# Kernel optimization log

Measured on AMD Instinct MI355X. Metric: run time of the kernel, lower is better.

Reference implementation:

```python
import jax, jax.numpy as jnp
import numpy as np

B, T, N, C = 1, 8, 1152, 768
H, DH = 12, 64          # attention heads / head dim; also RG-LRU block-diagonal heads
MLP = 3072
LRU = 768
CONV_W = 4              # recurrentgemma temporal conv width
N_IMG = 1024            # image tokens blocked by mask_image2image


def rms_norm(x, scale):
    var = jnp.mean(jnp.square(x), axis=-1, keepdims=True)
    return x * jax.lax.rsqrt(var + 1e-6) * (1.0 + scale)


def layer_norm(x, scale, bias):
    m = jnp.mean(x, axis=-1, keepdims=True)
    v = jnp.var(x, axis=-1, keepdims=True)
    return (x - m) * jax.lax.rsqrt(v + 1e-6) * scale + bias


def block_diag_linear(x, w, b):
    # x [..., LRU] -> per-head block-diagonal linear (recurrentgemma BlockDiagonalLinear)
    xs = x.reshape(x.shape[:-1] + (H, DH))
    y = jnp.einsum('...hd,hde->...he', xs, w) + b
    return y.reshape(x.shape)


def setup_inputs():
    key = jax.random.key(0)
    ks = jax.random.split(key, 24)
    def nrm(k, shape, s=0.02):
        return jax.random.normal(k, shape, jnp.float32) * s
    return dict(
        x=jax.random.normal(ks[0], (B, T, N, C), jnp.float32),
        tpre_scale=nrm(ks[1], (C,)),
        w_y=nrm(ks[2], (C, LRU)), b_y=jnp.zeros((LRU,)),
        w_x=nrm(ks[3], (C, LRU)), b_x=jnp.zeros((LRU,)),
        conv_w=nrm(ks[4], (CONV_W, LRU)), conv_b=jnp.zeros((LRU,)),
        a_param=jax.random.uniform(ks[5], (LRU,), jnp.float32, 1.0, 4.0),
        ig_w=nrm(ks[6], (H, DH, DH)), ig_b=jnp.zeros((H, DH)),
        ag_w=nrm(ks[7], (H, DH, DH)), ag_b=jnp.zeros((H, DH)),
        w_out=nrm(ks[8], (LRU, C)), b_out=jnp.zeros((C,)),
        cpre_scale=nrm(ks[9], (C,)),
        ffw_up_w=nrm(ks[10], (2, C, MLP)), ffw_up_b=jnp.zeros((2, MLP)),
        ffw_down_w=nrm(ks[11], (MLP, C)), ffw_down_b=jnp.zeros((C,)),
        ln1_s=jnp.ones((C,)), ln1_b=jnp.zeros((C,)),
        wq=nrm(ks[12], (C, H, DH)), bq=jnp.zeros((H, DH)),
        wk=nrm(ks[13], (C, H, DH)), bk=jnp.zeros((H, DH)),
        wv=nrm(ks[14], (C, H, DH)), bv=jnp.zeros((H, DH)),
        wo=nrm(ks[15], (H, DH, C)), bo=jnp.zeros((C,)),
        ln2_s=jnp.ones((C,)), ln2_b=jnp.zeros((C,)),
        mlp_w1=nrm(ks[16], (C, MLP)), mlp_b1=jnp.zeros((MLP,)),
        mlp_w2=nrm(ks[17], (MLP, C)), mlp_b2=jnp.zeros((C,)),
    )


def forward(x, tpre_scale, w_y, b_y, w_x, b_x, conv_w, conv_b, a_param,
            ig_w, ig_b, ag_w, ag_b, w_out, b_out, cpre_scale,
            ffw_up_w, ffw_up_b, ffw_down_w, ffw_down_b,
            ln1_s, ln1_b, wq, bq, wk, bk, wv, bv, wo, bo,
            ln2_s, ln2_b, mlp_w1, mlp_b1, mlp_w2, mlp_b2):
    b, t, n, c = x.shape
    # ---- temporal RG-LRU residual block over time: [(b t) n c] -> [(b n) t c] ----
    xt = x.transpose(0, 2, 1, 3).reshape(b * n, t, c)
    raw = xt
    xn = rms_norm(xt, tpre_scale)
    y = jax.nn.gelu(xn @ w_y + b_y)              # gate branch
    u = xn @ w_x + b_x                           # recurrent branch
    # causal depthwise temporal conv (width 4)
    up = jnp.pad(u, ((0, 0), (CONV_W - 1, 0), (0, 0)))
    u = sum(conv_w[i] * up[:, i:i + t] for i in range(CONV_W)) + conv_b
    # RG-LRU
    gate_x = jax.nn.sigmoid(block_diag_linear(u, ig_w, ig_b))
    gate_a = jax.nn.sigmoid(block_diag_linear(u, ag_w, ag_b))
    log_a = -8.0 * gate_a * jax.nn.softplus(a_param)
    a = jnp.exp(log_a)                           # [bn, t, LRU]
    mult = jnp.sqrt(jnp.maximum(1.0 - jnp.exp(2.0 * log_a), 0.0))
    reset = (jnp.arange(t) == 0)[None, :, None]
    mult = jnp.where(reset, 1.0, mult)
    a = jnp.where(reset, 0.0, a)
    norm_x = u * gate_x * mult
    def step(h, inputs):
        a_t, x_t = inputs
        h = a_t * h + x_t
        return h, h
    _, hs = jax.lax.scan(step, jnp.zeros((b * n, LRU), u.dtype),
                         (a.transpose(1, 0, 2), norm_x.transpose(1, 0, 2)))
    h = hs.transpose(1, 0, 2)                    # [bn, t, LRU]
    s = (h * y) @ w_out + b_out
    resid = s + raw
    # gated MLP (recurrentgemma MLPBlock)
    z = rms_norm(resid, cpre_scale)
    up2 = jnp.einsum('btd,cdD->cbtD', z, ffw_up_w) + ffw_up_b[:, None, None, :]
    z = (jax.nn.gelu(up2[0]) * up2[1]) @ ffw_down_w + ffw_down_b
    xt = z + resid
    # ---- spatial ViT block over tokens: back to [(b t) n c] ----
    xs = xt.reshape(b, n, t, c).transpose(0, 2, 1, 3).reshape(b * t, n, c)
    y1 = layer_norm(xs, ln1_s, ln1_b)
    q = jnp.einsum('bnc,chd->bnhd', y1, wq) + bq
    k = jnp.einsum('bnc,chd->bnhd', y1, wk) + bk
    v = jnp.einsum('bnc,chd->bnhd', y1, wv) + bv
    logits = jnp.einsum('bqhd,bkhd->bhqk', q, k) / jnp.sqrt(jnp.asarray(DH, q.dtype))
    # mask_image2image: image tokens (first 1024) cannot attend to image tokens
    mask = jnp.ones((n, n), bool).at[:N_IMG, :N_IMG].set(False)
    logits = jnp.where(mask[None, None], logits, jnp.finfo(logits.dtype).min)
    attn = jax.nn.softmax(logits, axis=-1)
    sa = jnp.einsum('bhqk,bkhd->bqhd', attn, v)
    sa = jnp.einsum('bqhd,hdc->bqc', sa, wo) + bo
    xs = xs + sa
    y2 = layer_norm(xs, ln2_s, ln2_b)
    m = jax.nn.gelu(y2 @ mlp_w1 + mlp_b1) @ mlp_w2 + mlp_b2
    xs = xs + m
    return xs.reshape(b, t, n, c)


def reference(x, tpre_scale, w_y, b_y, w_x, b_x, conv_w, conv_b, a_param,
              ig_w, ig_b, ag_w, ag_b, w_out, b_out, cpre_scale,
              ffw_up_w, ffw_up_b, ffw_down_w, ffw_down_b,
              ln1_s, ln1_b, wq, bq, wk, bk, wv, bv, wo, bo,
              ln2_s, ln2_b, mlp_w1, mlp_b1, mlp_w2, mlp_b2):
    return forward(x, tpre_scale, w_y, b_y, w_x, b_x, conv_w, conv_b, a_param,
                   ig_w, ig_b, ag_w, ag_b, w_out, b_out, cpre_scale,
                   ffw_up_w, ffw_up_b, ffw_down_w, ffw_down_b,
                   ln1_s, ln1_b, wq, bq, wk, bk, wv, bv, wo, bo,
                   ln2_s, ln2_b, mlp_w1, mlp_b1, mlp_w2, mlp_b2)
```

## Files before the change

kernel.cpp:

```cpp
#include <hip/hip_runtime.h>
#include <hip/hip_bf16.h>

typedef __hip_bfloat16 bf16;
typedef __attribute__((ext_vector_type(4))) float f32x4;
typedef __attribute__((ext_vector_type(8))) short short8;
typedef __attribute__((ext_vector_type(4))) short s16x4;

#define T_ 8
#define N_ 1152
#define C_ 768
#define H_ 12
#define DH_ 64
#define MLP_ 3072
#define LRU_ 768
#define NIMG_ 1024
#define M_ (T_*N_)

__device__ __forceinline__ float b2f(bf16 v){ return __bfloat162float(v); }
__device__ __forceinline__ bf16  f2b(float f){ return __float2bfloat16(f); }
__device__ __forceinline__ float bfs(short u){ return __uint_as_float(((unsigned int)(unsigned short)u) << 16); }
__device__ __forceinline__ float gelu_tanh(float x){
  float x3 = x*x*x;
  float z = 1.5957691216057308f*(x + 0.044715f*x3);
  float e = __expf(z);
  float t = 1.f - 2.f/(e + 1.f);
  return 0.5f*x*(1.f + t);
}
__device__ __forceinline__ void gll16(const void* g, void* l) {
  __builtin_amdgcn_global_load_lds((const __attribute__((address_space(1))) void*)g,
                                   (__attribute__((address_space(3))) void*)l, 16, 0, 0);
}
__device__ __forceinline__ f32x4 mfma16(short8 a, short8 b, f32x4 c) {
  return __builtin_amdgcn_mfma_f32_16x16x32_bf16(a, b, c, 0, 0, 0);
}

__global__ __launch_bounds__(256)
void convertT(const float* __restrict__ W, bf16* __restrict__ Wt, int Kd, int Nd,
              int rs, int ro) {
  __shared__ float tile[64][65];
  int k0 = blockIdx.y * 64, n0 = blockIdx.x * 64;
  int tid = threadIdx.x;
  int c = tid & 63, rr = tid >> 6;
  #pragma unroll
  for (int i = 0; i < 16; i++) {
    int r = rr * 16 + i;
    tile[r][c] = W[(size_t)(k0 + r) * Nd + n0 + c];
  }
  __syncthreads();
  #pragma unroll
  for (int i = 0; i < 16; i++) {
    int n = rr * 16 + i;
    Wt[(size_t)((n0 + n) * rs + ro) * Kd + k0 + c] = f2b(tile[c][n]);
  }
}

struct CvJob  { const float* src; bf16* dst; };
struct CvJobs { CvJob j[4]; };
__global__ __launch_bounds__(256)
void convertT4(CvJobs jobs, int Kd, int Nd, int rs, int zro) {
  __shared__ float tile[64][65];
  int z = blockIdx.z;
  const float* __restrict__ W  = jobs.j[z].src;
  bf16* __restrict__ Wt        = jobs.j[z].dst;
  int ro = z * zro;
  int k0 = blockIdx.y * 64, n0 = blockIdx.x * 64;
  int tid = threadIdx.x;
  int c = tid & 63, rr = tid >> 6;
  #pragma unroll
  for (int i = 0; i < 16; i++) {
    int r = rr * 16 + i;
    tile[r][c] = W[(size_t)(k0 + r) * Nd + n0 + c];
  }
  __syncthreads();
  #pragma unroll
  for (int i = 0; i < 16; i++) {
    int n = rr * 16 + i;
    Wt[(size_t)((n0 + n) * rs + ro) * Kd + k0 + c] = f2b(tile[c][n]);
  }
}

__global__ __launch_bounds__(256)
void convert_gw(const float* __restrict__ igw, const float* __restrict__ agw,
                const float* __restrict__ igb, const float* __restrict__ agb,
                bf16* __restrict__ GW, float* __restrict__ GB) {
  int h = blockIdx.x;
  for (int idx = threadIdx.x; idx < 128 * 64; idx += 256) {
    int rowc = idx >> 6;
    int d    = idx & 63;
    int e    = rowc >> 1;
    const float* W = (rowc & 1) ? agw : igw;
    GW[((size_t)h * 128 + rowc) * 64 + d] = f2b(W[((size_t)h * 64 + d) * 64 + e]);
  }
  if (threadIdx.x < 128) {
    int rowc = threadIdx.x;
    GB[h * 128 + rowc] = ((rowc & 1) ? agb : igb)[h * 64 + (rowc >> 1)];
  }
}

template<int EPI, int ACT>
__global__ __launch_bounds__(256)
void mgemm(const bf16* __restrict__ A, const bf16* __restrict__ Wt,
           const float* __restrict__ bias, const float* __restrict__ bias2,
           void* __restrict__ outp, int K, int Nd) {
  __shared__ bf16 As[2][128][32];
  __shared__ bf16 Bs[2][128][32];
  int tid = threadIdx.x;
  int wave = tid >> 6, lane = tid & 63;
  int wm = wave >> 1, wn = wave & 1;
  int ln15 = lane & 15, quad = lane >> 4;
  int row0 = blockIdx.y * 128, col0 = blockIdx.x * 128;
  const bf16* ag = A  + (size_t)(row0 + wave*32 + (lane>>2)) * K + (lane&3)*8;
  const bf16* bg = Wt + (size_t)(col0 + wave*32 + (lane>>2)) * K + (lane&3)*8;
  f32x4 zero = {0.f, 0.f, 0.f, 0.f};
  f32x4 acc[4][4];
  #pragma unroll
  for (int i = 0; i < 4; i++)
    #pragma unroll
    for (int j = 0; j < 4; j++) acc[i][j] = zero;

  gll16(ag,          &As[0][wave*32][0]);
  gll16(ag + 16*K,   &As[0][wave*32 + 16][0]);
  gll16(bg,          &Bs[0][wave*32][0]);
  gll16(bg + 16*K,   &Bs[0][wave*32 + 16][0]);
  __syncthreads();

  int nt = K >> 5;
  int cur = 0;
  for (int t = 0; t < nt; ++t) {
    if (t + 1 < nt) {
      int k1 = (t + 1) << 5;
      gll16(ag + k1,          &As[cur^1][wave*32][0]);
      gll16(ag + 16*K + k1,   &As[cur^1][wave*32 + 16][0]);
      gll16(bg + k1,          &Bs[cur^1][wave*32][0]);
      gll16(bg + 16*K + k1,   &Bs[cur^1][wave*32 + 16][0]);
    }
    short8 af[4], bf[4];
    #pragma unroll
    for (int i = 0; i < 4; i++)
      af[i] = *(const short8*)&As[cur][wm*64 + i*16 + ln15][quad*8];
    #pragma unroll
    for (int i = 0; i < 4; i++)
      bf[i] = *(const short8*)&Bs[cur][wn*64 + i*16 + ln15][quad*8];
    #pragma unroll
    for (int i = 0; i < 4; i++)
      #pragma unroll
      for (int j = 0; j < 4; j++)
        acc[i][j] = mfma16(af[i], bf[j], acc[i][j]);
    __syncthreads();
    cur ^= 1;
  }

  #pragma unroll
  for (int i = 0; i < 4; i++) {
    #pragma unroll
    for (int j = 0; j < 4; j++) {
      int col = col0 + wn*64 + j*16 + ln15;
      float bv;
      if (EPI == 3)      bv = bias[(col & 1) * (Nd >> 1) + (col >> 1)];
      else if (EPI == 4) bv = (col < (Nd >> 1)) ? bias[col] : bias2[col - (Nd >> 1)];
      else               bv = bias[col];
      #pragma unroll
      for (int r = 0; r < 4; r++) {
        int row = row0 + wm*64 + i*16 + quad*4 + r;
        float v = acc[i][j][r] + bv;
        if (EPI == 3) {
          float pv = __shfl_xor(v, 1, 64);
          if ((lane & 1) == 0)
            ((bf16*)outp)[(size_t)row * (Nd >> 1) + (col >> 1)] = f2b(gelu_tanh(v) * pv);
        } else if (EPI == 4) {
          if (ACT && col < (Nd >> 1)) v = gelu_tanh(v);
          ((bf16*)outp)[(size_t)row * Nd + col] = f2b(v);
        } else {
          if (ACT) v = gelu_tanh(v);
          if (EPI == 0) {
            ((bf16*)outp)[(size_t)row * Nd + col] = f2b(v);
          } else if (EPI == 1) {
            size_t o = (size_t)row * Nd + col;
            ((float*)outp)[o] = v + bias2[o];
          } else if (EPI == 2) {
            int tt = row / N_; int nn = row - tt * N_;
            ((bf16*)outp)[(((size_t)tt * H_ + (col >> 6)) * 64 + (col & 63)) * N_ + nn] = f2b(v);
          }
        }
      }
    }
  }
}

template<int LN>
__global__ __launch_bounds__(256)
void norm_kernel(const float* __restrict__ inp, const float* __restrict__ s,
                 const float* __restrict__ b, bf16* __restrict__ out) {
  int wid  = threadIdx.x >> 6;
  int lane = threadIdx.x & 63;
  int tok  = blockIdx.x * 4 + wid;
  const float* ip = inp + (size_t)tok*C_ + lane*4;
  f32x4 v[3];
  float sum = 0.f, sq = 0.f;
  #pragma unroll
  for (int i = 0; i < 3; i++) {
    v[i] = *(const f32x4*)(ip + i*256);
    #pragma unroll
    for (int j = 0; j < 4; j++) { sum += v[i][j]; sq += v[i][j]*v[i][j]; }
  }
  #pragma unroll
  for (int o = 32; o > 0; o >>= 1) {
    sum += __shfl_xor(sum, o, 64);
    sq  += __shfl_xor(sq, o, 64);
  }
  float scale, mean = 0.f;
  if (LN) {
    mean = sum * (1.f / C_);
    float var = sq * (1.f / C_) - mean * mean;
    scale = rsqrtf(var + 1e-6f);
  } else {
    scale = rsqrtf(sq * (1.f / C_) + 1e-6f);
  }
  #pragma unroll
  for (int i = 0; i < 3; i++) {
    int c0 = i*256 + lane*4;
    f32x4 sc = *(const f32x4*)(s + c0);
    f32x4 bb;
    if (LN) bb = *(const f32x4*)(b + c0);
    bf16 tmp[4];
    #pragma unroll
    for (int j = 0; j < 4; j++) {
      float r;
      if (LN) r = (v[i][j] - mean) * scale * sc[j] + bb[j];
      else    r = v[i][j] * scale * (1.f + sc[j]);
      tmp[j] = f2b(r);
    }
    *(s16x4*)(out + (size_t)tok*C_ + c0) = *(const s16x4*)tmp;
  }
}

__global__ __launch_bounds__(256)
void conv_kernel(const bf16* __restrict__ u0, const float* __restrict__ cw,
                 const float* __restrict__ cb, bf16* __restrict__ uc, int us, int uo) {
  int idx = blockIdx.x * 256 + threadIdx.x;
  int c8  = idx % (LRU_/8);
  int tok = idx / (LRU_/8);
  int ch0 = c8 * 8;
  int n = tok % N_;
  int t = tok / N_;
  float acc[8];
  {
    f32x4 b0 = *(const f32x4*)(cb + ch0);
    f32x4 b1 = *(const f32x4*)(cb + ch0 + 4);
    #pragma unroll
    for (int j = 0; j < 4; j++) { acc[j] = b0[j]; acc[4+j] = b1[j]; }
  }
  #pragma unroll
  for (int i = 0; i < 4; i++) {
    int tt = t - 3 + i;
    if (tt >= 0) {
      short8 v = *(const short8*)&u0[(size_t)(tt*N_ + n)*us + uo + ch0];
      f32x4 w0 = *(const f32x4*)(cw + i*LRU_ + ch0);
      f32x4 w1 = *(const f32x4*)(cw + i*LRU_ + ch0 + 4);
      #pragma unroll
      for (int j = 0; j < 4; j++) {
        acc[j]   += w0[j] * bfs(v[j]);
        acc[4+j] += w1[j] * bfs(v[4+j]);
      }
    }
  }
  bf16 tmp[8];
  #pragma unroll
  for (int j = 0; j < 8; j++) tmp[j] = f2b(acc[j]);
  *(short8*)&uc[(size_t)tok*LRU_ + ch0] = *(const short8*)tmp;
}

__global__ __launch_bounds__(256)
void gates_mfma(const bf16* __restrict__ uc, const bf16* __restrict__ GW,
                const float* __restrict__ GB, const float* __restrict__ ap,
                bf16* __restrict__ a_out, bf16* __restrict__ nx_out) {
  __shared__ bf16 As[128][64];
  __shared__ bf16 Bs[128][64];
  int tid = threadIdx.x;
  int wave = tid >> 6, lane = tid & 63;
  int wm = wave >> 1, wn = wave & 1;
  int ln15 = lane & 15, quad = lane >> 4;
  int row0 = blockIdx.x * 128;
  int h = blockIdx.y;
  #pragma unroll
  for (int i = 0; i < 4; i++) {
    int chunk = wave * 4 + i;
    gll16(uc + (size_t)(row0 + chunk*8 + (lane>>3)) * LRU_ + h*DH_ + (lane&7)*8,
          &As[chunk*8][0]);
    gll16(GW + (size_t)h*128*64 + chunk*512 + lane*8, &Bs[chunk*8][0]);
  }
  __syncthreads();
  f32x4 zero = {0.f, 0.f, 0.f, 0.f};
  f32x4 acc[4][4];
  #pragma unroll
  for (int i = 0; i < 4; i++)
    #pragma unroll
    for (int j = 0; j < 4; j++) acc[i][j] = zero;
  short8 af0[4], af1[4], bf0[4], bf1[4];
  #pragma unroll
  for (int i = 0; i < 4; i++) {
    af0[i] = *(const short8*)&As[wm*64 + i*16 + ln15][quad*8];
    af1[i] = *(const short8*)&As[wm*64 + i*16 + ln15][32 + quad*8];
    bf0[i] = *(const short8*)&Bs[wn*64 + i*16 + ln15][quad*8];
    bf1[i] = *(const short8*)&Bs[wn*64 + i*16 + ln15][32 + quad*8];
  }
  #pragma unroll
  for (int i = 0; i < 4; i++)
    #pragma unroll
    for (int j = 0; j < 4; j++) {
      acc[i][j] = mfma16(af0[i], bf0[j], acc[i][j]);
      acc[i][j] = mfma16(af1[i], bf1[j], acc[i][j]);
    }
  __syncthreads();

  int t_is0 = (row0 < N_);
  int odd = lane & 1;
  float bvj[4], spj[4];
  #pragma unroll
  for (int j = 0; j < 4; j++) {
    int col = wn*64 + j*16 + ln15;
    bvj[j] = GB[h*128 + col];
    int e = col >> 1;
    float apv = ap[h*DH_ + e];
    spj[j] = (apv > 20.f) ? apv : log1pf(__expf(apv));
  }
  #pragma unroll
  for (int i = 0; i < 4; i++) {
    #pragma unroll
    for (int j = 0; j < 4; j++) {
      int col = wn*64 + j*16 + ln15;
      int e = col >> 1;
      #pragma unroll
      for (int r = 0; r < 4; r++) {
        int lr = wm*64 + i*16 + quad*4 + r;
        float v = acc[i][j][r] + bvj[j];
        float g = 1.f / (1.f + __expf(-v));
        float mult = 1.f;
        if (odd) {
          float log_a = -8.f * g * spj[j];
          float a = __expf(log_a);
          mult = sqrtf(fmaxf(1.f - a*a, 0.f));
          if (t_is0) { a = 0.f; mult = 1.f; }
          Bs[lr][e] = f2b(a);
        }
        float mp = __shfl_xor(mult, 1, 64);
        if (!odd) {
          float uv = b2f(As[lr][e]);
          As[lr][e] = f2b(uv * g * mp);
        }
      }
    }
  }
  __syncthreads();
  int rr = tid >> 3, cc = (tid & 7) * 8;
  #pragma unroll
  for (int it = 0; it < 4; it++) {
    int row = it * 32 + rr;
    size_t o = (size_t)(row0 + row) * LRU_ + h*DH_ + cc;
    *(short8*)(nx_out + o) = *(const short8*)&As[row][cc];
    *(short8*)(a_out  + o) = *(const short8*)&Bs[row][cc];
  }
}

__global__ __launch_bounds__(256)
void scan_kernel(const bf16* __restrict__ a, const bf16* __restrict__ nx,
                 const bf16* __restrict__ y, bf16* __restrict__ hy, int ys) {
  int idx = blockIdx.x * 256 + threadIdx.x;
  int c8 = idx % (LRU_/8);
  int n  = idx / (LRU_/8);
  int ch0 = c8 * 8;
  float h[8] = {0.f,0.f,0.f,0.f,0.f,0.f,0.f,0.f};
  #pragma unroll
  for (int t = 0; t < T_; t++) {
    size_t p = (size_t)(t*N_ + n) * LRU_ + ch0;
    short8 av = *(const short8*)(a + p);
    short8 nv = *(const short8*)(nx + p);
    short8 yv = *(const short8*)(y + (size_t)(t*N_ + n) * ys + ch0);
    bf16 tmp[8];
    #pragma unroll
    for (int j = 0; j < 8; j++) {
      h[j] = bfs(av[j]) * h[j] + bfs(nv[j]);
      tmp[j] = f2b(h[j] * bfs(yv[j]));
    }
    *(short8*)(hy + p) = *(const short8*)tmp;
  }
}

__global__ __launch_bounds__(256)
void fattn(const bf16* __restrict__ QK, const bf16* __restrict__ Vt,
           bf16* __restrict__ O) {
  __shared__ bf16 Ks[128][64];
  __shared__ bf16 VTs[64][128];
  __shared__ bf16 Ps[4][16][128];
  int qb = blockIdx.x, th = blockIdx.y;
  int h = th % H_, t = th / H_;
  int wave = threadIdx.x >> 6, lane = threadIdx.x & 63;
  int ln15 = lane & 15, quad = lane >> 4;
  int q0, kv0, nch;
  if (qb < 16) { q0 = qb * 64;            kv0 = NIMG_; nch = 1; }
  else         { q0 = NIMG_ + (qb-16)*64; kv0 = 0;     nch = 9; }
  int qw = q0 + wave * 16;
  const bf16* qp = QK + (size_t)(t*N_ + qw + ln15) * 1536 + h*DH_ + quad*8;
  short8 aq0 = *(const short8*)qp;
  short8 aq1 = *(const short8*)(qp + 32);
  f32x4 zero = {0.f, 0.f, 0.f, 0.f};
  f32x4 oacc[4];
  #pragma unroll
  for (int d = 0; d < 4; d++) oacc[d] = zero;
  float mi[4], li[4];
  #pragma unroll
  for (int r = 0; r < 4; r++) { mi[r] = -1e30f; li[r] = 0.f; }

  for (int ch = 0; ch < nch; ch++) {
    int kb = t*N_ + kv0 + ch*128;
    #pragma unroll
    for (int i = 0; i < 4; i++) {
      int r = wave*32 + i*8;
      gll16(QK + (size_t)(kb + r + (lane>>3))*1536 + 768 + h*DH_ + (lane&7)*8, &Ks[r][0]);
    }
    #pragma unroll
    for (int i = 0; i < 4; i++) {
      int d = wave*16 + i*4;
      gll16(Vt + ((size_t)(t*H_ + h)*64 + d + (lane>>4))*N_ + kv0 + ch*128 + ln15*8,
            &VTs[d][0]);
    }
    __syncthreads();
    f32x4 s[8];
    #pragma unroll
    for (int nt = 0; nt < 8; nt++) {
      short8 b0 = *(const short8*)&Ks[nt*16 + ln15][quad*8];
      short8 b1 = *(const short8*)&Ks[nt*16 + ln15][32 + quad*8];
      f32x4 c_ = zero;
      c_ = mfma16(aq0, b0, c_);
      c_ = mfma16(aq1, b1, c_);
      #pragma unroll
      for (int r = 0; r < 4; r++) s[nt][r] = c_[r] * 0.125f;
    }
    float alpha[4], lsum[4];
    #pragma unroll
    for (int r = 0; r < 4; r++) {
      float m_ = s[0][r];
      #pragma unroll
      for (int nt = 1; nt < 8; nt++) m_ = fmaxf(m_, s[nt][r]);
      #pragma unroll
      for (int o = 1; o < 16; o <<= 1) m_ = fmaxf(m_, __shfl_xor(m_, o, 64));
      float mnew = fmaxf(mi[r], m_);
      alpha[r] = __expf(mi[r] - mnew);
      mi[r] = mnew;
      lsum[r] = 0.f;
    }
    #pragma unroll
    for (int nt = 0; nt < 8; nt++)
      #pragma unroll
      for (int r = 0; r < 4; r++) {
        float p = __expf(s[nt][r] - mi[r]);
        s[nt][r] = p; lsum[r] += p;
      }
    #pragma unroll
    for (int r = 0; r < 4; r++) {
      float l_ = lsum[r];
      #pragma unroll
      for (int o = 1; o < 16; o <<= 1) l_ += __shfl_xor(l_, o, 64);
      li[r] = li[r] * alpha[r] + l_;
    }
    #pragma unroll
    for (int nt = 0; nt < 8; nt++)
      #pragma unroll
      for (int r = 0; r < 4; r++)
        Ps[wave][quad*4 + r][nt*16 + ln15] = f2b(s[nt][r]);
    #pragma unroll
    for (int d = 0; d < 4; d++)
      #pragma unroll
      for (int r = 0; r < 4; r++) oacc[d][r] *= alpha[r];
    #pragma unroll
    for (int ks = 0; ks < 4; ks++) {
      short8 pa = *(const short8*)&Ps[wave][ln15][ks*32 + quad*8];
      #pragma unroll
      for (int dt = 0; dt < 4; dt++) {
        short8 vb = *(const short8*)&VTs[dt*16 + ln15][ks*32 + quad*8];
        oacc[dt] = mfma16(pa, vb, oacc[dt]);
      }
    }
    __syncthreads();
  }
  #pragma unroll
  for (int dt = 0; dt < 4; dt++)
    #pragma unroll
    for (int r = 0; r < 4; r++)
      O[(size_t)(t*N_ + qw + quad*4 + r)*C_ + h*DH_ + dt*16 + ln15]
        = f2b(oacc[dt][r] / li[r]);
}

extern "C" void kernel_launch(void* const* d_in, const int* in_sizes, int n_in,
                              void* d_out, int out_size, void* d_ws, size_t ws_size,
                              hipStream_t stream) {
  (void)in_sizes; (void)n_in; (void)out_size; (void)ws_size;
  const float* x        = (const float*)d_in[0];
  const float* tpre     = (const float*)d_in[1];
  const float* w_y      = (const float*)d_in[2];
  const float* b_y      = (const float*)d_in[3];
  const float* w_x      = (const float*)d_in[4];
  const float* b_x      = (const float*)d_in[5];
  const float* conv_w   = (const float*)d_in[6];
  const float* conv_b   = (const float*)d_in[7];
  const float* a_param  = (const float*)d_in[8];
  const float* ig_w     = (const float*)d_in[9];
  const float* ig_b     = (const float*)d_in[10];
  const float* ag_w     = (const float*)d_in[11];
  const float* ag_b     = (const float*)d_in[12];
  const float* w_out    = (const float*)d_in[13];
  const float* b_out    = (const float*)d_in[14];
  const float* cpre     = (const float*)d_in[15];
  const float* ffw_up_w = (const float*)d_in[16];
  const float* ffw_up_b = (const float*)d_in[17];
  const float* ffw_dn_w = (const float*)d_in[18];
  const float* ffw_dn_b = (const float*)d_in[19];
  const float* ln1_s    = (const float*)d_in[20];
  const float* ln1_b    = (const float*)d_in[21];
  const float* wq       = (const float*)d_in[22];
  const float* bq       = (const float*)d_in[23];
  const float* wk       = (const float*)d_in[24];
  const float* bk       = (const float*)d_in[25];
  const float* wv       = (const float*)d_in[26];
  const float* bv       = (const float*)d_in[27];
  const float* wo       = (const float*)d_in[28];
  const float* bo       = (const float*)d_in[29];
  const float* ln2_s    = (const float*)d_in[30];
  const float* ln2_b    = (const float*)d_in[31];
  const float* mlp_w1   = (const float*)d_in[32];
  const float* mlp_b1   = (const float*)d_in[33];
  const float* mlp_w2   = (const float*)d_in[34];
  const float* mlp_b2   = (const float*)d_in[35];

  const size_t MC = (size_t)M_ * C_;
  const size_t W68 = (size_t)C_ * C_;
  const size_t WUP = (size_t)C_ * MLP_;
  bf16* B0 = (bf16*)d_ws;
  bf16* B1 = B0 + MC;
  bf16* B2 = B1 + MC;
  bf16* BV = B2 + MC;
  float* F0 = (float*)(BV + MC);
  float* F1 = F0 + MC;
  bf16* F0b = (bf16*)F0;
  bf16* B0b = (bf16*)B0;
  float* xsF = (float*)B0;
  float* outF = (float*)d_out;
  bf16*  GW = (bf16*)F1;
  float* GB = (float*)(GW + (size_t)H_*128*64);
  bf16*  WtO = F0b + 3*MC;

  dim3 blk(256);
  dim3 gN768(C_/128, M_/128);
  dim3 g1536(1536/128, M_/128);
  dim3 cvUp(48, 12);
  dim3 cvDn(12, 48);

  {
    CvJobs j1 = {{{w_y, BV}, {w_x, BV + W68}, {w_out, WtO}, {w_y, BV}}};
    convertT4<<<dim3(12, 12, 3), blk, 0, stream>>>(j1, C_, C_, 1, 0);
  }
  convert_gw<<<H_, blk, 0, stream>>>(ig_w, ag_w, ig_b, ag_b, GW, GB);
  norm_kernel<0><<<M_/4, blk, 0, stream>>>(x, tpre, nullptr, B0);
  mgemm<4,1><<<g1536, blk, 0, stream>>>(B0, BV, b_y, b_x, F0b, C_, 1536);
  conv_kernel<<<(M_*(LRU_/8))/256, blk, 0, stream>>>(F0b, conv_w, conv_b, B1, 1536, 768);
  gates_mfma<<<dim3(M_/128, H_), blk, 0, stream>>>(B1, GW, GB, a_param, B2, BV);
  scan_kernel<<<(N_*(LRU_/8))/256, blk, 0, stream>>>(B2, BV, F0b, B0, 1536);
  mgemm<1,0><<<gN768, blk, 0, stream>>>(B0, WtO, b_out, x, outF, C_, C_);

  norm_kernel<0><<<M_/4, blk, 0, stream>>>(outF, cpre, nullptr, B0);
  {
    CvJobs j2 = {{{ffw_up_w, B1}, {ffw_up_w + WUP, B1}, {ffw_up_w, B1}, {ffw_up_w, B1}}};
    convertT4<<<dim3(48, 12, 2), blk, 0, stream>>>(j2, C_, MLP_, 2, 1);
  }
  convertT<<<cvDn, blk, 0, stream>>>(ffw_dn_w, BV, MLP_, C_, 1, 0);
  {
    dim3 gUp(6144/128, M_/128);
    dim3 gDn(C_/128,   M_/128);
    mgemm<3,0><<<gUp, blk, 0, stream>>>(B0, B1, ffw_up_b, nullptr, F0b, C_, 6144);
    mgemm<1,0><<<gDn, blk, 0, stream>>>(F0b, BV, ffw_dn_b, outF, xsF, MLP_, C_);
  }

  norm_kernel<1><<<M_/4, blk, 0, stream>>>(xsF, ln1_s, ln1_b, B2);
  {
    CvJobs j3 = {{{wq, BV}, {wk, BV + W68}, {wv, BV + 2*W68}, {wo, BV + 3*W68}}};
    convertT4<<<dim3(12, 12, 4), blk, 0, stream>>>(j3, C_, C_, 1, 0);
  }
  mgemm<4,0><<<g1536, blk, 0, stream>>>(B2, BV, bq, bk, F0b, C_, 1536);
  mgemm<2,0><<<gN768, blk, 0, stream>>>(B2, BV + 2*W68, bv, nullptr, F0b + 2*MC, C_, C_);
  fattn<<<dim3(18, T_*H_), blk, 0, stream>>>(F0b, F0b + 2*MC, B2);
  mgemm<1,0><<<gN768, blk, 0, stream>>>(B2, BV + 3*W68, bo, xsF, outF, C_, C_);
  norm_kernel<1><<<M_/4, blk, 0, stream>>>(outF, ln2_s, ln2_b, B2);
  convertT<<<cvUp, blk, 0, stream>>>(mlp_w1, B0b,       C_, MLP_, 1, 0);
  convertT<<<cvDn, blk, 0, stream>>>(mlp_w2, B0b + WUP, MLP_, C_, 1, 0);
  {
    dim3 gM1(MLP_/128, M_/128);
    dim3 gM2(C_/128,   M_/128);
    mgemm<0,1><<<gM1, blk, 0, stream>>>(B2, B0b, mlp_b1, nullptr, F0b, C_, MLP_);
    mgemm<1,0><<<gM2, blk, 0, stream>>>(F0b, B0b + WUP, mlp_b2, outF, outF, MLP_, C_);
  }
}
```

Before: 906.7 us.

## Fuse temporal conv into gates kernel and add XCD-aware block swizzle

The standalone temporal conv kernel is removed. Its 4-tap convolution is computed inside gates_mfma while the A tile is filled in shared memory, so the intermediate conv buffer no longer makes a global round trip and one launch is gone. Separately, an XCD swizzle remaps flat block IDs in mgemm, gates and flash attention so that neighbouring tiles land on the same chiplet, aiming at better L2 reuse. The fused path reads four input taps per row directly from global memory, and the swizzle assumes the block count is divisible by 8.

```diff
diff --git a/kernel.cpp b/kernel.cpp
--- a/kernel.cpp
+++ b/kernel.cpp
@@ -32,6 +32,9 @@
 }
 __device__ __forceinline__ f32x4 mfma16(short8 a, short8 b, f32x4 c) {
   return __builtin_amdgcn_mfma_f32_16x16x32_bf16(a, b, c, 0, 0, 0);
+}
+__device__ __forceinline__ int xcd_swz(int flat, int nwg) {
+  return (flat & 7) * (nwg >> 3) + (flat >> 3);
 }
 
 __global__ __launch_bounds__(256)
@@ -108,7 +111,8 @@
   int wave = tid >> 6, lane = tid & 63;
   int wm = wave >> 1, wn = wave & 1;
   int ln15 = lane & 15, quad = lane >> 4;
-  int row0 = blockIdx.y * 128, col0 = blockIdx.x * 128;
+  int nf = xcd_swz(blockIdx.y * gridDim.x + blockIdx.x, gridDim.x * gridDim.y);
+  int row0 = (nf / gridDim.x) * 128, col0 = (nf % gridDim.x) * 128;
   const bf16* ag = A  + (size_t)(row0 + wave*32 + (lane>>2)) * K + (lane&3)*8;
   const bf16* bg = Wt + (size_t)(col0 + wave*32 + (lane>>2)) * K + (lane&3)*8;
   f32x4 zero = {0.f, 0.f, 0.f, 0.f};
@@ -235,43 +239,8 @@
 }
 
 __global__ __launch_bounds__(256)
-void conv_kernel(const bf16* __restrict__ u0, const float* __restrict__ cw,
-                 const float* __restrict__ cb, bf16* __restrict__ uc, int us, int uo) {
-  int idx = blockIdx.x * 256 + threadIdx.x;
-  int c8  = idx % (LRU_/8);
-  int tok = idx / (LRU_/8);
-  int ch0 = c8 * 8;
-  int n = tok % N_;
-  int t = tok / N_;
-  float acc[8];
-  {
-    f32x4 b0 = *(const f32x4*)(cb + ch0);
-    f32x4 b1 = *(const f32x4*)(cb + ch0 + 4);
-    #pragma unroll
-    for (int j = 0; j < 4; j++) { acc[j] = b0[j]; acc[4+j] = b1[j]; }
-  }
-  #pragma unroll
-  for (int i = 0; i < 4; i++) {
-    int tt = t - 3 + i;
-    if (tt >= 0) {
-      short8 v = *(const short8*)&u0[(size_t)(tt*N_ + n)*us + uo + ch0];
-      f32x4 w0 = *(const f32x4*)(cw + i*LRU_ + ch0);
-      f32x4 w1 = *(const f32x4*)(cw + i*LRU_ + ch0 + 4);
-      #pragma unroll
-      for (int j = 0; j < 4; j++) {
-        acc[j]   += w0[j] * bfs(v[j]);
-        acc[4+j] += w1[j] * bfs(v[4+j]);
-      }
-    }
-  }
-  bf16 tmp[8];
-  #pragma unroll
-  for (int j = 0; j < 8; j++) tmp[j] = f2b(acc[j]);
-  *(short8*)&uc[(size_t)tok*LRU_ + ch0] = *(const short8*)tmp;
-}
-
-__global__ __launch_bounds__(256)
-void gates_mfma(const bf16* __restrict__ uc, const bf16* __restrict__ GW,
+void gates_mfma(const bf16* __restrict__ yu, const float* __restrict__ cw,
+                const float* __restrict__ cb, const bf16* __restrict__ GW,
                 const float* __restrict__ GB, const float* __restrict__ ap,
                 bf16* __restrict__ a_out, bf16* __restrict__ nx_out) {
   __shared__ bf16 As[128][64];
@@ -280,14 +249,41 @@
   int wave = tid >> 6, lane = tid & 63;
   int wm = wave >> 1, wn = wave & 1;
   int ln15 = lane & 15, quad = lane >> 4;
-  int row0 = blockIdx.x * 128;
-  int h = blockIdx.y;
+  int nf = xcd_swz(blockIdx.y * gridDim.x + blockIdx.x, gridDim.x * gridDim.y);
+  int bx = nf % 72, h = nf / 72;
+  int row0 = bx * 128;
+  int tt0   = bx / 9;
+  int nbase = (bx % 9) * 128;
+  int rin = lane >> 3, colblk = lane & 7, ch0 = colblk * 8;
+  f32x4 cb0 = *(const f32x4*)(cb + h*DH_ + ch0);
+  f32x4 cb1 = *(const f32x4*)(cb + h*DH_ + ch0 + 4);
   #pragma unroll
   for (int i = 0; i < 4; i++) {
     int chunk = wave * 4 + i;
-    gll16(uc + (size_t)(row0 + chunk*8 + (lane>>3)) * LRU_ + h*DH_ + (lane&7)*8,
-          &As[chunk*8][0]);
     gll16(GW + (size_t)h*128*64 + chunk*512 + lane*8, &Bs[chunk*8][0]);
+    int row = chunk*8 + rin;
+    int n = nbase + row;
+    float acc8[8];
+    #pragma unroll
+    for (int j = 0; j < 4; j++) { acc8[j] = cb0[j]; acc8[4+j] = cb1[j]; }
+    #pragma unroll
+    for (int tap = 0; tap < 4; tap++) {
+      int tt = tt0 - 3 + tap;
+      if (tt >= 0) {
+        short8 v = *(const short8*)&yu[(size_t)(tt*N_ + n)*1536 + 768 + h*DH_ + ch0];
+        f32x4 w0 = *(const f32x4*)(cw + tap*LRU_ + h*DH_ + ch0);
+        f32x4 w1 = *(const f32x4*)(cw + tap*LRU_ + h*DH_ + ch0 + 4);
+        #pragma unroll
+        for (int j = 0; j < 4; j++) {
+          acc8[j]   += w0[j] * bfs(v[j]);
+          acc8[4+j] += w1[j] * bfs(v[4+j]);
+        }
+      }
+    }
+    bf16 tmp[8];
+    #pragma unroll
+    for (int j = 0; j < 8; j++) tmp[j] = f2b(acc8[j]);
+    *(short8*)&As[row][ch0] = *(const short8*)tmp;
   }
   __syncthreads();
   f32x4 zero = {0.f, 0.f, 0.f, 0.f};
@@ -313,7 +309,7 @@
     }
   __syncthreads();
 
-  int t_is0 = (row0 < N_);
+  int t_is0 = (tt0 == 0);
   int odd = lane & 1;
   float bvj[4], spj[4];
   #pragma unroll
@@ -392,7 +388,8 @@
   __shared__ bf16 Ks[128][64];
   __shared__ bf16 VTs[64][128];
   __shared__ bf16 Ps[4][16][128];
-  int qb = blockIdx.x, th = blockIdx.y;
+  int nf = xcd_swz(blockIdx.y * gridDim.x + blockIdx.x, gridDim.x * gridDim.y);
+  int qb = nf % 18, th = nf / 18;
   int h = th % H_, t = th / H_;
   int wave = threadIdx.x >> 6, lane = threadIdx.x & 63;
   int ln15 = lane & 15, quad = lane >> 4;
@@ -562,8 +559,8 @@
   convert_gw<<<H_, blk, 0, stream>>>(ig_w, ag_w, ig_b, ag_b, GW, GB);
   norm_kernel<0><<<M_/4, blk, 0, stream>>>(x, tpre, nullptr, B0);
   mgemm<4,1><<<g1536, blk, 0, stream>>>(B0, BV, b_y, b_x, F0b, C_, 1536);
-  conv_kernel<<<(M_*(LRU_/8))/256, blk, 0, stream>>>(F0b, conv_w, conv_b, B1, 1536, 768);
-  gates_mfma<<<dim3(M_/128, H_), blk, 0, stream>>>(B1, GW, GB, a_param, B2, BV);
+  gates_mfma<<<dim3(72, H_), blk, 0, stream>>>(F0b, conv_w, conv_b, GW, GB,
+                                               a_param, B2, BV);
   scan_kernel<<<(N_*(LRU_/8))/256, blk, 0, stream>>>(B2, BV, F0b, B0, 1536);
   mgemm<1,0><<<gN768, blk, 0, stream>>>(B0, WtO, b_out, x, outF, C_, C_);
 
```

Measured after the change: 885.7 us. -2.3%, faster.
